# Kernel optimization log

Measured on AMD Instinct MI355X. Metric: run time of the kernel, lower is better.

## Reference

```python
import jax, jax.numpy as jnp
import numpy as np

N_NODES = 50000
N_EDGES = 800000
IN_DIM = 5
HID = (32, 64, 128, 64, 32)
OUT_DIM = 2
EPS = 1e-5  # nn.BatchNorm1d default eps


def _bn(x, g, b):
    # BatchNorm1d in training mode: batch (biased) statistics over nodes
    m = jnp.mean(x, axis=0)
    v = jnp.var(x, axis=0)
    return (x - m) * jax.lax.rsqrt(v + EPS) * g + b


def setup_inputs() -> dict:
    key = jax.random.key(0)
    ks = jax.random.split(key, 40)
    it = iter(range(40))
    def nrm(shape, s=0.1):
        return jax.random.normal(ks[next(it)], shape, jnp.float32) * s
    inp = {}
    inp["x"] = jax.random.normal(ks[next(it)], (N_NODES, IN_DIM), jnp.float32)
    inp["edge_index"] = jax.random.randint(ks[next(it)], (2, N_EDGES), 0, N_NODES, jnp.int32)
    # input embedding: Linear(5,32) -> ReLU -> BatchNorm1d(32)
    inp["emb_W"] = nrm((IN_DIM, HID[0]))
    inp["emb_b"] = jnp.zeros((HID[0],), jnp.float32)
    inp["emb_g"] = jnp.ones((HID[0],), jnp.float32)
    inp["emb_beta"] = jnp.zeros((HID[0],), jnp.float32)
    # 4 GraphConv blocks
    for i in range(len(HID) - 1):
        din, dout = HID[i], HID[i + 1]
        inp[f"b{i}_Wrel"] = nrm((din, dout))   # lin_rel weight (has bias)
        inp[f"b{i}_brel"] = jnp.zeros((dout,), jnp.float32)
        inp[f"b{i}_Wroot"] = nrm((din, dout))  # lin_root weight (no bias)
        inp[f"b{i}_g"] = jnp.ones((dout,), jnp.float32)
        inp[f"b{i}_beta"] = jnp.zeros((dout,), jnp.float32)
    # output MLP: Linear(32,16) -> ReLU -> Linear(16,2)
    inp["out_W1"] = nrm((HID[-1], HID[-1] // 2))
    inp["out_b1"] = jnp.zeros((HID[-1] // 2,), jnp.float32)
    inp["out_W2"] = nrm((HID[-1] // 2, OUT_DIM))
    inp["out_b2"] = jnp.zeros((OUT_DIM,), jnp.float32)
    return inp


def reference(x, edge_index,
              emb_W, emb_b, emb_g, emb_beta,
              b0_Wrel, b0_brel, b0_Wroot, b0_g, b0_beta,
              b1_Wrel, b1_brel, b1_Wroot, b1_g, b1_beta,
              b2_Wrel, b2_brel, b2_Wroot, b2_g, b2_beta,
              b3_Wrel, b3_brel, b3_Wroot, b3_g, b3_beta,
              out_W1, out_b1, out_W2, out_b2):
    src, dst = edge_index[0], edge_index[1]
    # input embedding: Linear -> ReLU -> BN
    h = jnp.maximum(x @ emb_W + emb_b, 0.0)
    h = _bn(h, emb_g, emb_beta)
    blocks = [
        (b0_Wrel, b0_brel, b0_Wroot, b0_g, b0_beta),
        (b1_Wrel, b1_brel, b1_Wroot, b1_g, b1_beta),
        (b2_Wrel, b2_brel, b2_Wroot, b2_g, b2_beta),
        (b3_Wrel, b3_brel, b3_Wroot, b3_g, b3_beta),
    ]
    for Wrel, brel, Wroot, g, beta in blocks:
        # GraphConv (aggr='add'): lin_rel(sum_{j in N(i)} x_j) + lin_root(x_i)
        agg = jax.ops.segment_sum(h[src], dst, num_segments=N_NODES)
        h = agg @ Wrel + brel + h @ Wroot
        # BN then ReLU (GNNBlock order)
        h = jnp.maximum(_bn(h, g, beta), 0.0)
    # output MLP
    h = jnp.maximum(h @ out_W1 + out_b1, 0.0)
    return h @ out_W2 + out_b2
```

## Files before the change

kernel.cpp:

```cpp
#include <hip/hip_runtime.h>

#define N_NODES 50000
#define N_EDGES 800000
#define BN_EPS 1e-5f

typedef unsigned int   u32;
typedef unsigned short u16;

__device__ __forceinline__ void fma4(float4& a, float s, const float4& w) {
    a.x += s * w.x; a.y += s * w.y; a.z += s * w.z; a.w += s * w.w;
}
__device__ __forceinline__ void add4(float4& a, const float4& b) {
    a.x += b.x; a.y += b.y; a.z += b.z; a.w += b.w;
}
__device__ __forceinline__ u16 f2bf(float f) {
    union { u32 i; float f; } c; c.f = f;
    return (u16)((c.i + 0x7FFFu + ((c.i >> 16) & 1u)) >> 16);
}
__device__ __forceinline__ float4 bf4(uint2 w) {
    union { u32 i; float f; } a, b, c, d;
    a.i = w.x << 16; b.i = w.x & 0xFFFF0000u;
    c.i = w.y << 16; d.i = w.y & 0xFFFF0000u;
    return make_float4(a.f, b.f, c.f, d.f);
}
__device__ __forceinline__ uint2 pack4(const float4& v) {
    uint2 w;
    w.x = (u32)f2bf(v.x) | ((u32)f2bf(v.y) << 16);
    w.y = (u32)f2bf(v.z) | ((u32)f2bf(v.w) << 16);
    return w;
}
__device__ __forceinline__ float bfx(const uint4& v, int kk) {
    u32 w = ((const u32*)&v)[kk >> 1];
    union { u32 i; float f; } c;
    c.i = (kk & 1) ? (w & 0xFFFF0000u) : (w << 16);
    return c.f;
}

template <int NY>
__device__ __forceinline__ bool xcd_decode(int nx, int& x, int& y) {
    const int s = blockIdx.x & (8 * NY - 1);
    const int g = blockIdx.x / (8 * NY);
    x = g * 8 + (s & 7);
    y = s >> 3;
    return x < nx;
}
static inline int xcd_grid(int nx, int ny) { return ((nx + 7) / 8 * 8) * ny; }

__global__ void zero_i(int* __restrict__ p, int n) {
    int i = blockIdx.x * blockDim.x + threadIdx.x;
    int stride = gridDim.x * blockDim.x;
    for (; i < n; i += stride) p[i] = 0;
}

__global__ void hist_kernel(const int* __restrict__ dst, int* __restrict__ cnt) {
    int i = blockIdx.x * blockDim.x + threadIdx.x;
    int stride = gridDim.x * blockDim.x;
    for (; i < N_EDGES; i += stride) atomicAdd(&cnt[dst[i]], 1);
}
__global__ void scan1_kernel(const int* __restrict__ cnt, int* __restrict__ rp,
                             int* __restrict__ bsum) {
    __shared__ int s[256];
    int t = threadIdx.x;
    int idx = blockIdx.x * 256 + t;
    int v = (idx < N_NODES) ? cnt[idx] : 0;
    s[t] = v;
    __syncthreads();
    for (int off = 1; off < 256; off <<= 1) {
        int x = 0;
        if (t >= off) x = s[t - off];
        __syncthreads();
        s[t] += x;
        __syncthreads();
    }
    if (idx < N_NODES) rp[idx] = s[t] - v;
    if (t == 255) bsum[blockIdx.x] = s[255];
}
__global__ void scan2_kernel(int* __restrict__ bsum, int nb, float* __restrict__ stats) {
    __shared__ int s[256];
    int t = threadIdx.x;
    for (int i = t; i < 5 * 256; i += 256) stats[i] = 0.f;
    int v = (t < nb) ? bsum[t] : 0;
    s[t] = v;
    __syncthreads();
    for (int off = 1; off < 256; off <<= 1) {
        int x = 0;
        if (t >= off) x = s[t - off];
        __syncthreads();
        s[t] += x;
        __syncthreads();
    }
    if (t < nb) bsum[t] = s[t] - v;
}
__global__ void scan3_kernel(int* __restrict__ rp, const int* __restrict__ bsum,
                             int* __restrict__ cnt) {
    int idx = blockIdx.x * 256 + threadIdx.x;
    if (idx < N_NODES) {
        rp[idx] += bsum[blockIdx.x];
        cnt[idx] = 0;
    }
    if (idx == 0) rp[N_NODES] = N_EDGES;
}
__global__ void fill_kernel(const int* __restrict__ src, const int* __restrict__ dst,
                            const int* __restrict__ rp, int* __restrict__ cur,
                            u16* __restrict__ ssrc) {
    int i = blockIdx.x * blockDim.x + threadIdx.x;
    int stride = gridDim.x * blockDim.x;
    for (; i < N_EDGES; i += stride) {
        int d = dst[i];
        int p = rp[d] + atomicAdd(&cur[d], 1);
        ssrc[p] = (u16)src[i];
    }
}

__global__ __launch_bounds__(256) void emb_fused(
    const float* __restrict__ x, const float* __restrict__ W,
    const float* __restrict__ b, u16* __restrict__ out16,
    float* __restrict__ stats) {
    __shared__ float lsum[32], lssq[32];
    if (threadIdx.x < 32) { lsum[threadIdx.x] = 0.f; lssq[threadIdx.x] = 0.f; }
    __syncthreads();
    const int o = threadIdx.x & 31;
    const int total = N_NODES * 32;
    float mys = 0.f, myq = 0.f;
    for (int base = blockIdx.x * 256; base < total; base += gridDim.x * 256) {
        int idx = base + threadIdx.x;
        float acc = 0.f;
        if (idx < total) {
            int n = idx >> 5;
            const float* xr = x + n * 5;
            acc = b[o];
#pragma unroll
            for (int k = 0; k < 5; ++k) acc += xr[k] * W[k * 32 + o];
            acc = fmaxf(acc, 0.f);
            out16[idx] = f2bf(acc);
        }
        mys += acc;
        myq += acc * acc;
    }
    mys += __shfl_xor(mys, 32);
    myq += __shfl_xor(myq, 32);
    if ((threadIdx.x & 63) < 32) { atomicAdd(&lsum[o], mys); atomicAdd(&lssq[o], myq); }
    __syncthreads();
    if (threadIdx.x < 32) {
        atomicAdd(&stats[threadIdx.x], lsum[threadIdx.x]);
        atomicAdd(&stats[32 + threadIdx.x], lssq[threadIdx.x]);
    }
}

template <int D>
__device__ __forceinline__ void bn_finalize_lds(
    const float* __restrict__ stats, const float* __restrict__ g,
    const float* __restrict__ beta, float* sc, float* sh) {
    const float invN = 1.f / (float)N_NODES;
    for (int f = threadIdx.x; f < D; f += 256) {
        float m = stats[f] * invN;
        float var = stats[D + f] * invN - m * m;
        float a = g[f] * rsqrtf(var + BN_EPS);
        sc[f] = a;
        sh[f] = beta[f] - m * a;
    }
    __syncthreads();
}

__global__ __launch_bounds__(256) void bn_apply16(
    const uint2* __restrict__ in16, u16* __restrict__ out16,
    const float* __restrict__ g, const float* __restrict__ beta,
    const float* __restrict__ stats, int logD) {
    const int D = 1 << logD;
    const int total4 = N_NODES << (logD - 2);
    const float invN = 1.f / (float)N_NODES;
    int idx = blockIdx.x * blockDim.x + threadIdx.x;
    int stride = gridDim.x * blockDim.x;
    for (; idx < total4; idx += stride) {
        int f = (idx & ((D >> 2) - 1)) << 2;
        float4 v = bf4(in16[idx]);
        float* vp = (float*)&v;
#pragma unroll
        for (int c = 0; c < 4; ++c) {
            float m = stats[f + c] * invN;
            float var = stats[D + f + c] * invN - m * m;
            vp[c] = fmaxf((vp[c] - m) * rsqrtf(var + BN_EPS) * g[f + c] + beta[f + c], 0.f);
        }
        ((uint2*)out16)[idx] = pack4(v);
    }
}

template <int LOGD>
__global__ __launch_bounds__(256) void gather_agg_bf16(
    const u16* __restrict__ h16, const int* __restrict__ rp,
    const u16* __restrict__ ssrc, uint2* __restrict__ agg16) {
    constexpr int QSH = LOGD - 2;
    int tid = blockIdx.x * 256 + threadIdx.x;
    int node = tid >> QSH;
    if (node >= N_NODES) return;
    int q = tid & ((1 << QSH) - 1);
    int e0 = rp[node], e1 = rp[node + 1];
    float4 acc = make_float4(0.f, 0.f, 0.f, 0.f);
    int e = e0;
    for (; e + 4 <= e1; e += 4) {
        int s0 = ssrc[e], s1 = ssrc[e + 1], s2 = ssrc[e + 2], s3 = ssrc[e + 3];
        uint2 w0 = ((const uint2*)(h16 + ((size_t)s0 << LOGD)))[q];
        uint2 w1 = ((const uint2*)(h16 + ((size_t)s1 << LOGD)))[q];
        uint2 w2 = ((const uint2*)(h16 + ((size_t)s2 << LOGD)))[q];
        uint2 w3 = ((const uint2*)(h16 + ((size_t)s3 << LOGD)))[q];
        float4 v0 = bf4(w0), v1 = bf4(w1), v2 = bf4(w2), v3 = bf4(w3);
        add4(v0, v1); add4(v2, v3); add4(acc, v0); add4(acc, v2);
    }
    for (; e < e1; ++e) {
        float4 v = bf4(((const uint2*)(h16 + ((size_t)ssrc[e] << LOGD)))[q]);
        add4(acc, v);
    }
    agg16[tid] = pack4(acc);
}

template <int DIN, int DOUT, int OBL, int NPT>
__global__ __launch_bounds__(256) void gconv_bn0(
    const u16* __restrict__ h16, const u16* __restrict__ agg16,
    const float* __restrict__ Wrel, const float* __restrict__ brel,
    const float* __restrict__ Wroot, u16* __restrict__ out16,
    const float* __restrict__ stats_in, const float* __restrict__ g_in,
    const float* __restrict__ beta_in, const int* __restrict__ deg,
    float* __restrict__ stats_out, int nx) {
    constexpr int NY = 2;
    constexpr int LPN = OBL / 4;
    constexpr int SLOTS = 256 / LPN;
    constexpr int KS = 8;
    constexpr int TOT4 = DIN * OBL / 4;
    int bx, by;
    if (!xcd_decode<NY>(nx, bx, by)) return;
    __shared__ __align__(16) float wl[2 * DIN * OBL];
    __shared__ __align__(16) float sc[DIN];
    __shared__ __align__(16) float sh[DIN];
    __shared__ float lsum[OBL], lssq[OBL];
    const int ob0 = by * OBL;
    for (int e4 = threadIdx.x; e4 < TOT4; e4 += 256) {
        int k = e4 / (OBL / 4);
        int j = (e4 % (OBL / 4)) * 4;
        ((float4*)wl)[e4] = *(const float4*)(Wrel + (size_t)k * DOUT + ob0 + j);
        ((float4*)wl)[TOT4 + e4] = *(const float4*)(Wroot + (size_t)k * DOUT + ob0 + j);
    }
    if (threadIdx.x < OBL) { lsum[threadIdx.x] = 0.f; lssq[threadIdx.x] = 0.f; }
    bn_finalize_lds<DIN>(stats_in, g_in, beta_in, sc, sh);

    const int q = threadIdx.x & (LPN - 1);
    const int slot = threadIdx.x / LPN;
    const int o0 = ob0 + q * 4;
    const int nbase = bx * (SLOTS * NPT) + slot;

    float degf[NPT];
#pragma unroll
    for (int i = 0; i < NPT; ++i) {
        int n = nbase + i * SLOTS;
        degf[i] = (n < N_NODES) ? (float)deg[n] : 0.f;
    }

    float4 bias = *(const float4*)(brel + o0);
    float4 acc[NPT];
#pragma unroll
    for (int i = 0; i < NPT; ++i) acc[i] = bias;

#pragma unroll 1
    for (int s = 0; s < DIN / KS; ++s) {
        const int k0 = s * KS;
        float4 s2[2] = {((const float4*)sc)[k0 / 4], ((const float4*)sc)[k0 / 4 + 1]};
        float4 t2[2] = {((const float4*)sh)[k0 / 4], ((const float4*)sh)[k0 / 4 + 1]};
        const float* scp = (const float*)s2;
        const float* shp = (const float*)t2;
        uint4 hv16[NPT], av16[NPT];
#pragma unroll
        for (int i = 0; i < NPT; ++i) {
            int n = nbase + i * SLOTS;
            int nn = (n < N_NODES) ? n : 0;
            hv16[i] = *(const uint4*)(h16 + (size_t)nn * DIN + k0);
            av16[i] = *(const uint4*)(agg16 + (size_t)nn * DIN + k0);
        }
#pragma unroll
        for (int kk = 0; kk < KS; ++kk) {
            float4 wr = *(const float4*)&wl[(k0 + kk) * OBL + q * 4];
            float4 wo = *(const float4*)&wl[DIN * OBL + (k0 + kk) * OBL + q * 4];
#pragma unroll
            for (int i = 0; i < NPT; ++i) {
                float a  = fmaf(bfx(av16[i], kk), scp[kk], degf[i] * shp[kk]);
                float hh = fmaf(bfx(hv16[i], kk), scp[kk], shp[kk]);
                fma4(acc[i], a, wr);
                fma4(acc[i], hh, wo);
            }
        }
    }
#pragma unroll
    for (int i = 0; i < NPT; ++i) {
        int n = nbase + i * SLOTS;
        if (n < N_NODES)
            *(uint2*)(out16 + (size_t)n * DOUT + o0) = pack4(acc[i]);
        else
            acc[i] = make_float4(0.f, 0.f, 0.f, 0.f);
    }
    float4 s4 = make_float4(0.f, 0.f, 0.f, 0.f);
    float4 q4 = make_float4(0.f, 0.f, 0.f, 0.f);
#pragma unroll
    for (int i = 0; i < NPT; ++i) {
        s4.x += acc[i].x; s4.y += acc[i].y; s4.z += acc[i].z; s4.w += acc[i].w;
        q4.x += acc[i].x * acc[i].x; q4.y += acc[i].y * acc[i].y;
        q4.z += acc[i].z * acc[i].z; q4.w += acc[i].w * acc[i].w;
    }
#pragma unroll
    for (int d = LPN; d < 64; d <<= 1) {
        s4.x += __shfl_xor(s4.x, d); s4.y += __shfl_xor(s4.y, d);
        s4.z += __shfl_xor(s4.z, d); s4.w += __shfl_xor(s4.w, d);
        q4.x += __shfl_xor(q4.x, d); q4.y += __shfl_xor(q4.y, d);
        q4.z += __shfl_xor(q4.z, d); q4.w += __shfl_xor(q4.w, d);
    }
    if ((threadIdx.x & 63) < LPN) {
        int c = q * 4;
        atomicAdd(&lsum[c + 0], s4.x); atomicAdd(&lsum[c + 1], s4.y);
        atomicAdd(&lsum[c + 2], s4.z); atomicAdd(&lsum[c + 3], s4.w);
        atomicAdd(&lssq[c + 0], q4.x); atomicAdd(&lssq[c + 1], q4.y);
        atomicAdd(&lssq[c + 2], q4.z); atomicAdd(&lssq[c + 3], q4.w);
    }
    __syncthreads();
    if (threadIdx.x < OBL) {
        atomicAdd(&stats_out[ob0 + threadIdx.x], lsum[threadIdx.x]);
        atomicAdd(&stats_out[DOUT + ob0 + threadIdx.x], lssq[threadIdx.x]);
    }
}

template <int DIN, int DOUT, int OBL, int NPT>
__global__ __launch_bounds__(256) void gconv_lds(
    const u16* __restrict__ h16, const u16* __restrict__ agg16,
    const float* __restrict__ Wrel, const float* __restrict__ brel,
    const float* __restrict__ Wroot, u16* __restrict__ out16,
    float* __restrict__ stats_out, int nx) {
    constexpr int NY = DOUT / OBL;
    constexpr int LPN = OBL / 4;
    constexpr int SLOTS = 256 / LPN;
    constexpr int KS = 8;
    constexpr int TOT4 = DIN * OBL / 4;
    int bx, by;
    if (!xcd_decode<NY>(nx, bx, by)) return;
    __shared__ __align__(16) float wl[2 * DIN * OBL];
    __shared__ float lsum[OBL], lssq[OBL];
    const int ob0 = by * OBL;
    for (int e4 = threadIdx.x; e4 < TOT4; e4 += 256) {
        int k = e4 / (OBL / 4);
        int j = (e4 % (OBL / 4)) * 4;
        ((float4*)wl)[e4] = *(const float4*)(Wrel + (size_t)k * DOUT + ob0 + j);
        ((float4*)wl)[TOT4 + e4] = *(const float4*)(Wroot + (size_t)k * DOUT + ob0 + j);
    }
    if (threadIdx.x < OBL) { lsum[threadIdx.x] = 0.f; lssq[threadIdx.x] = 0.f; }
    __syncthreads();

    const int q = threadIdx.x & (LPN - 1);
    const int slot = threadIdx.x / LPN;
    const int o0 = ob0 + q * 4;
    const int nbase = bx * (SLOTS * NPT) + slot;

    float4 bias = *(const float4*)(brel + o0);
    float4 acc[NPT];
#pragma unroll
    for (int i = 0; i < NPT; ++i) acc[i] = bias;

#pragma unroll 1
    for (int s = 0; s < DIN / KS; ++s) {
        const int k0 = s * KS;
        uint4 hv16[NPT], av16[NPT];
#pragma unroll
        for (int i = 0; i < NPT; ++i) {
            int n = nbase + i * SLOTS;
            int nn = (n < N_NODES) ? n : 0;
            hv16[i] = *(const uint4*)(h16 + (size_t)nn * DIN + k0);
            av16[i] = *(const uint4*)(agg16 + (size_t)nn * DIN + k0);
        }
#pragma unroll
        for (int kk = 0; kk < KS; ++kk) {
            float4 wr = *(const float4*)&wl[(k0 + kk) * OBL + q * 4];
            float4 wo = *(const float4*)&wl[DIN * OBL + (k0 + kk) * OBL + q * 4];
#pragma unroll
            for (int i = 0; i < NPT; ++i) {
                fma4(acc[i], bfx(av16[i], kk), wr);
                fma4(acc[i], bfx(hv16[i], kk), wo);
            }
        }
    }
#pragma unroll
    for (int i = 0; i < NPT; ++i) {
        int n = nbase + i * SLOTS;
        if (n < N_NODES)
            *(uint2*)(out16 + (size_t)n * DOUT + o0) = pack4(acc[i]);
        else
            acc[i] = make_float4(0.f, 0.f, 0.f, 0.f);
    }
    float4 s4 = make_float4(0.f, 0.f, 0.f, 0.f);
    float4 q4 = make_float4(0.f, 0.f, 0.f, 0.f);
#pragma unroll
    for (int i = 0; i < NPT; ++i) {
        s4.x += acc[i].x; s4.y += acc[i].y; s4.z += acc[i].z; s4.w += acc[i].w;
        q4.x += acc[i].x * acc[i].x; q4.y += acc[i].y * acc[i].y;
        q4.z += acc[i].z * acc[i].z; q4.w += acc[i].w * acc[i].w;
    }
#pragma unroll
    for (int d = LPN; d < 64; d <<= 1) {
        s4.x += __shfl_xor(s4.x, d); s4.y += __shfl_xor(s4.y, d);
        s4.z += __shfl_xor(s4.z, d); s4.w += __shfl_xor(s4.w, d);
        q4.x += __shfl_xor(q4.x, d); q4.y += __shfl_xor(q4.y, d);
        q4.z += __shfl_xor(q4.z, d); q4.w += __shfl_xor(q4.w, d);
    }
    if ((threadIdx.x & 63) < LPN) {
        int c = q * 4;
        atomicAdd(&lsum[c + 0], s4.x); atomicAdd(&lsum[c + 1], s4.y);
        atomicAdd(&lsum[c + 2], s4.z); atomicAdd(&lsum[c + 3], s4.w);
        atomicAdd(&lssq[c + 0], q4.x); atomicAdd(&lssq[c + 1], q4.y);
        atomicAdd(&lssq[c + 2], q4.z); atomicAdd(&lssq[c + 3], q4.w);
    }
    __syncthreads();
    if (threadIdx.x < OBL) {
        atomicAdd(&stats_out[ob0 + threadIdx.x], lsum[threadIdx.x]);
        atomicAdd(&stats_out[DOUT + ob0 + threadIdx.x], lssq[threadIdx.x]);
    }
}

template <int DIN, int DOUT, int OBL, int NPT>
__global__ __launch_bounds__(256) void prem_bn16(
    const u16* __restrict__ h16, const float* __restrict__ Wrel,
    const float* __restrict__ brel, const float* __restrict__ Wroot,
    u16* __restrict__ P16, float* __restrict__ Q,
    const float* __restrict__ stats_in, const float* __restrict__ g_in,
    const float* __restrict__ beta_in, int nx) {
    constexpr int NY = DOUT / OBL;
    constexpr int LPN = OBL / 4;
    constexpr int SLOTS = 256 / LPN;
    constexpr int KS = 8;
    constexpr int TOT4 = DIN * OBL / 4;
    int bx, by;
    if (!xcd_decode<NY>(nx, bx, by)) return;
    __shared__ __align__(16) float wl[2 * DIN * OBL];
    __shared__ __align__(16) float sc[DIN];
    __shared__ __align__(16) float sh[DIN];
    const int ob0 = by * OBL;
    for (int e4 = threadIdx.x; e4 < TOT4; e4 += 256) {
        int k = e4 / (OBL / 4);
        int j = (e4 % (OBL / 4)) * 4;
        ((float4*)wl)[e4] = *(const float4*)(Wrel + (size_t)k * DOUT + ob0 + j);
        ((float4*)wl)[TOT4 + e4] = *(const float4*)(Wroot + (size_t)k * DOUT + ob0 + j);
    }
    bn_finalize_lds<DIN>(stats_in, g_in, beta_in, sc, sh);

    const int q = threadIdx.x & (LPN - 1);
    const int slot = threadIdx.x / LPN;
    const int o0 = ob0 + q * 4;
    const int nbase = bx * (SLOTS * NPT) + slot;

    float4 bias = *(const float4*)(brel + o0);
    float4 accp[NPT], accq[NPT];
#pragma unroll
    for (int i = 0; i < NPT; ++i) {
        accp[i] = make_float4(0.f, 0.f, 0.f, 0.f);
        accq[i] = bias;
    }

#pragma unroll 1
    for (int s = 0; s < DIN / KS; ++s) {
        const int k0 = s * KS;
        float4 s2[2] = {((const float4*)sc)[k0 / 4], ((const float4*)sc)[k0 / 4 + 1]};
        float4 t2[2] = {((const float4*)sh)[k0 / 4], ((const float4*)sh)[k0 / 4 + 1]};
        const float* scp = (const float*)s2;
        const float* shp = (const float*)t2;
        uint4 hv16[NPT];
#pragma unroll
        for (int i = 0; i < NPT; ++i) {
            int n = nbase + i * SLOTS;
            int nn = (n < N_NODES) ? n : 0;
            hv16[i] = *(const uint4*)(h16 + (size_t)nn * DIN + k0);
        }
#pragma unroll
        for (int kk = 0; kk < KS; ++kk) {
            float4 wr = *(const float4*)&wl[(k0 + kk) * OBL + q * 4];
            float4 wo = *(const float4*)&wl[DIN * OBL + (k0 + kk) * OBL + q * 4];
#pragma unroll
            for (int i = 0; i < NPT; ++i) {
                float hh = fmaxf(fmaf(bfx(hv16[i], kk), scp[kk], shp[kk]), 0.f);
                fma4(accp[i], hh, wr);
                fma4(accq[i], hh, wo);
            }
        }
    }
#pragma unroll
    for (int i = 0; i < NPT; ++i) {
        int n = nbase + i * SLOTS;
        if (n < N_NODES) {
            *(uint2*)(P16 + (size_t)n * DOUT + o0) = pack4(accp[i]);
            *(float4*)(Q + (size_t)n * DOUT + o0) = accq[i];
        }
    }
}

template <int LOGD, int W16>
__global__ __launch_bounds__(256) void gather_add_bf16(
    const u16* __restrict__ P16, const int* __restrict__ rp,
    const u16* __restrict__ ssrc, float4* __restrict__ qio,
    u16* __restrict__ out16, float* __restrict__ stats) {
    constexpr int D = 1 << LOGD;
    constexpr int Q4 = D / 4;
    __shared__ float lsum[D], lssq[D];
    if (threadIdx.x < D) { lsum[threadIdx.x] = 0.f; lssq[threadIdx.x] = 0.f; }
    __syncthreads();

    const int total = N_NODES * Q4;
    const int q = threadIdx.x & (Q4 - 1);
    float4 mys = make_float4(0.f, 0.f, 0.f, 0.f);
    float4 myq = make_float4(0.f, 0.f, 0.f, 0.f);

    for (int base = blockIdx.x * 256; base < total; base += gridDim.x * 256) {
        int tid = base + threadIdx.x;
        float4 acc = make_float4(0.f, 0.f, 0.f, 0.f);
        if (tid < total) {
            int node = tid >> (LOGD - 2);
            int e0 = rp[node], e1 = rp[node + 1];
            acc = qio[tid];
            int e = e0;
            for (; e + 4 <= e1; e += 4) {
                int s0 = ssrc[e], s1 = ssrc[e + 1], s2 = ssrc[e + 2], s3 = ssrc[e + 3];
                uint2 w0 = ((const uint2*)(P16 + ((size_t)s0 << LOGD)))[q];
                uint2 w1 = ((const uint2*)(P16 + ((size_t)s1 << LOGD)))[q];
                uint2 w2 = ((const uint2*)(P16 + ((size_t)s2 << LOGD)))[q];
                uint2 w3 = ((const uint2*)(P16 + ((size_t)s3 << LOGD)))[q];
                float4 v0 = bf4(w0), v1 = bf4(w1), v2 = bf4(w2), v3 = bf4(w3);
                add4(v0, v1); add4(v2, v3); add4(acc, v0); add4(acc, v2);
            }
            for (; e < e1; ++e) {
                float4 v = bf4(((const uint2*)(P16 + ((size_t)ssrc[e] << LOGD)))[q]);
                add4(acc, v);
            }
            if (W16)
                ((uint2*)out16)[tid] = pack4(acc);
            else
                qio[tid] = acc;
        }
        mys.x += acc.x; mys.y += acc.y; mys.z += acc.z; mys.w += acc.w;
        myq.x += acc.x * acc.x; myq.y += acc.y * acc.y;
        myq.z += acc.z * acc.z; myq.w += acc.w * acc.w;
    }
#pragma unroll
    for (int d = Q4; d < 64; d <<= 1) {
        mys.x += __shfl_xor(mys.x, d); mys.y += __shfl_xor(mys.y, d);
        mys.z += __shfl_xor(mys.z, d); mys.w += __shfl_xor(mys.w, d);
        myq.x += __shfl_xor(myq.x, d); myq.y += __shfl_xor(myq.y, d);
        myq.z += __shfl_xor(myq.z, d); myq.w += __shfl_xor(myq.w, d);
    }
    if ((threadIdx.x & 63) < Q4) {
        atomicAdd(&lsum[4 * q + 0], mys.x); atomicAdd(&lsum[4 * q + 1], mys.y);
        atomicAdd(&lsum[4 * q + 2], mys.z); atomicAdd(&lsum[4 * q + 3], mys.w);
        atomicAdd(&lssq[4 * q + 0], myq.x); atomicAdd(&lssq[4 * q + 1], myq.y);
        atomicAdd(&lssq[4 * q + 2], myq.z); atomicAdd(&lssq[4 * q + 3], myq.w);
    }
    __syncthreads();
    if (threadIdx.x < D) {
        atomicAdd(&stats[threadIdx.x], lsum[threadIdx.x]);
        atomicAdd(&stats[D + threadIdx.x], lssq[threadIdx.x]);
    }
}

__global__ __launch_bounds__(256) void outmlp_kernel(
    const float* __restrict__ h, const float* __restrict__ stats,
    const float* __restrict__ g, const float* __restrict__ beta,
    const float* __restrict__ W1, const float* __restrict__ b1,
    const float* __restrict__ W2, const float* __restrict__ b2,
    float* __restrict__ out) {
    int n = blockIdx.x * 256 + threadIdx.x;
    if (n >= N_NODES) return;
    const float invN = 1.f / (float)N_NODES;
    const float4* hr4 = (const float4*)(h + (size_t)n * 32);
    float hv[32];
#pragma unroll
    for (int k4 = 0; k4 < 8; ++k4) {
        float4 v = hr4[k4];
        float* vp = (float*)&v;
#pragma unroll
        for (int c = 0; c < 4; ++c) {
            int f = 4 * k4 + c;
            float m = stats[f] * invN;
            float var = stats[32 + f] * invN - m * m;
            hv[f] = fmaxf((vp[c] - m) * rsqrtf(var + BN_EPS) * g[f] + beta[f], 0.f);
        }
    }
    float hid[16];
#pragma unroll
    for (int j = 0; j < 16; ++j) hid[j] = b1[j];
#pragma unroll
    for (int k = 0; k < 32; ++k) {
        float hk = hv[k];
#pragma unroll
        for (int j = 0; j < 16; ++j) hid[j] += hk * W1[k * 16 + j];
    }
    float o0 = b2[0], o1 = b2[1];
#pragma unroll
    for (int j = 0; j < 16; ++j) {
        float t = fmaxf(hid[j], 0.f);
        o0 += t * W2[j * 2 + 0];
        o1 += t * W2[j * 2 + 1];
    }
    out[n * 2 + 0] = o0;
    out[n * 2 + 1] = o1;
}

extern "C" void kernel_launch(void* const* d_in, const int* in_sizes, int n_in,
                              void* d_out, int out_size, void* d_ws, size_t ws_size,
                              hipStream_t stream) {
    const float* x        = (const float*)d_in[0];
    const int*   ei       = (const int*)d_in[1];
    const int*   src      = ei;
    const int*   dst      = ei + N_EDGES;
    const float* emb_W    = (const float*)d_in[2];
    const float* emb_b    = (const float*)d_in[3];
    const float* emb_g    = (const float*)d_in[4];
    const float* emb_beta = (const float*)d_in[5];
    const float* out_W1   = (const float*)d_in[26];
    const float* out_b1   = (const float*)d_in[27];
    const float* out_W2   = (const float*)d_in[28];
    const float* out_b2   = (const float*)d_in[29];

    float* ws = (float*)d_ws;
    float* q32   = ws;
    float* stats = ws + (size_t)N_NODES * 64;
    u16* h16emb = (u16*)(stats + 5 * 256);
    u16* AGG16  = h16emb + (size_t)N_NODES * 32;
    u16* r0_16  = AGG16 + (size_t)N_NODES * 64;
    u16* h16a   = r0_16 + (size_t)N_NODES * 64;
    u16* r1_16  = h16a + (size_t)N_NODES * 64;
    u16* h2_16  = r1_16 + (size_t)N_NODES * 128;
    int* rp     = (int*)(h2_16 + (size_t)N_NODES * 64);
    int* cnt    = rp + N_NODES + 1;
    int* bsum   = cnt + N_NODES;
    u16* ssrc   = (u16*)(bsum + 256);

    float* st0 = stats;
    float* st1 = stats + 256;
    float* st2 = stats + 512;
    float* st3 = stats + 768;
    float* st4 = stats + 1024;

    const int BS = 256;
    const int NB = (N_NODES + BS - 1) / BS;

    zero_i<<<64, BS, 0, stream>>>(cnt, N_NODES);
    hist_kernel<<<1024, BS, 0, stream>>>(dst, cnt);
    scan1_kernel<<<NB, 256, 0, stream>>>(cnt, rp, bsum);
    scan2_kernel<<<1, 256, 0, stream>>>(bsum, NB, stats);
    scan3_kernel<<<NB, 256, 0, stream>>>(rp, bsum, cnt);
    fill_kernel<<<1024, BS, 0, stream>>>(src, dst, rp, cnt, ssrc);

    emb_fused<<<512, BS, 0, stream>>>(x, emb_W, emb_b, h16emb, st0);

    gather_agg_bf16<5><<<(N_NODES * 8 + BS - 1) / BS, BS, 0, stream>>>(h16emb, rp, ssrc, (uint2*)AGG16);
    {
        const int nx = (N_NODES + 63) / 64;
        gconv_bn0<32, 64, 32, 2><<<xcd_grid(nx, 2), BS, 0, stream>>>(
            h16emb, AGG16, (const float*)d_in[6], (const float*)d_in[7], (const float*)d_in[8],
            r0_16, st0, emb_g, emb_beta, cnt, st1, nx);
    }
    bn_apply16<<<2048, BS, 0, stream>>>((const uint2*)r0_16, h16a,
                                        (const float*)d_in[9], (const float*)d_in[10], st1, 6);

    gather_agg_bf16<6><<<(N_NODES * 16 + BS - 1) / BS, BS, 0, stream>>>(h16a, rp, ssrc, (uint2*)AGG16);
    {
        const int nx = (N_NODES + 127) / 128;
        gconv_lds<64, 128, 32, 4><<<xcd_grid(nx, 4), BS, 0, stream>>>(
            h16a, AGG16, (const float*)d_in[11], (const float*)d_in[12], (const float*)d_in[13],
            r1_16, st2, nx);
    }

    {
        const int nx = (N_NODES + 127) / 128;
        prem_bn16<128, 64, 16, 2><<<xcd_grid(nx, 4), BS, 0, stream>>>(
            r1_16, (const float*)d_in[16], (const float*)d_in[17], (const float*)d_in[18],
            AGG16, q32, st2, (const float*)d_in[14], (const float*)d_in[15], nx);
    }
    gather_add_bf16<6, 1><<<512, BS, 0, stream>>>(AGG16, rp, ssrc, (float4*)q32, h2_16, st3);

    {
        const int nx = (N_NODES + 127) / 128;
        prem_bn16<64, 32, 16, 2><<<xcd_grid(nx, 2), BS, 0, stream>>>(
            h2_16, (const float*)d_in[21], (const float*)d_in[22], (const float*)d_in[23],
            AGG16, q32, st3, (const float*)d_in[19], (const float*)d_in[20], nx);
    }
    gather_add_bf16<5, 0><<<512, BS, 0, stream>>>(AGG16, rp, ssrc, (float4*)q32, (u16*)0, st4);

    outmlp_kernel<<<NB, BS, 0, stream>>>(
        q32, st4, (const float*)d_in[24], (const float*)d_in[25],
        out_W1, out_b1, out_W2, out_b2, (float*)d_out);
}
```

Baseline: 346.5 us.

## Fuse histogram with embedding kernel and enlarge gconv_bn0 row tile

Merges the edge-degree histogram and the input-embedding kernels into one launch, with disjoint block ranges doing each job, and moves the stats zeroing from scan2 into a combined zero kernel. The aim is to cut launch count and let the two independent jobs overlap on the GPU. It also changes gconv_bn0's template parameter from 2 to 4 and doubles the node tile from 64 to 128 rows, giving fewer, larger blocks. Risks: the gconv_bn0 tile change has to match the kernel's internal tiling assumptions, and the larger tile lowers the block count.

```diff
diff --git a/kernel.cpp b/kernel.cpp
--- a/kernel.cpp
+++ b/kernel.cpp
@@ -46,17 +46,59 @@
 }
 static inline int xcd_grid(int nx, int ny) { return ((nx + 7) / 8 * 8) * ny; }
 
-__global__ void zero_i(int* __restrict__ p, int n) {
-    int i = blockIdx.x * blockDim.x + threadIdx.x;
+__global__ void zero_all(int* __restrict__ cnt, float* __restrict__ stats) {
     int stride = gridDim.x * blockDim.x;
-    for (; i < n; i += stride) p[i] = 0;
-}
-
-__global__ void hist_kernel(const int* __restrict__ dst, int* __restrict__ cnt) {
-    int i = blockIdx.x * blockDim.x + threadIdx.x;
-    int stride = gridDim.x * blockDim.x;
-    for (; i < N_EDGES; i += stride) atomicAdd(&cnt[dst[i]], 1);
-}
+    for (int i = blockIdx.x * blockDim.x + threadIdx.x; i < N_NODES; i += stride)
+        cnt[i] = 0;
+    for (int i = blockIdx.x * blockDim.x + threadIdx.x; i < 5 * 256; i += stride)
+        stats[i] = 0.f;
+}
+
+#define HIST_BLOCKS 1024
+#define EMB_BLOCKS  512
+__global__ __launch_bounds__(256) void hist_emb_kernel(
+    const int* __restrict__ dst, int* __restrict__ cnt,
+    const float* __restrict__ x, const float* __restrict__ W,
+    const float* __restrict__ b, u16* __restrict__ out16,
+    float* __restrict__ stats) {
+    if (blockIdx.x < HIST_BLOCKS) {
+        int i = blockIdx.x * 256 + threadIdx.x;
+        int stride = HIST_BLOCKS * 256;
+        for (; i < N_EDGES; i += stride) atomicAdd(&cnt[dst[i]], 1);
+        return;
+    }
+    __shared__ float lsum[32], lssq[32];
+    if (threadIdx.x < 32) { lsum[threadIdx.x] = 0.f; lssq[threadIdx.x] = 0.f; }
+    __syncthreads();
+    const int o = threadIdx.x & 31;
+    const int total = N_NODES * 32;
+    const int ebid = blockIdx.x - HIST_BLOCKS;
+    float mys = 0.f, myq = 0.f;
+    for (int base = ebid * 256; base < total; base += EMB_BLOCKS * 256) {
+        int idx = base + threadIdx.x;
+        float acc = 0.f;
+        if (idx < total) {
+            int n = idx >> 5;
+            const float* xr = x + n * 5;
+            acc = b[o];
+#pragma unroll
+            for (int k = 0; k < 5; ++k) acc += xr[k] * W[k * 32 + o];
+            acc = fmaxf(acc, 0.f);
+            out16[idx] = f2bf(acc);
+        }
+        mys += acc;
+        myq += acc * acc;
+    }
+    mys += __shfl_xor(mys, 32);
+    myq += __shfl_xor(myq, 32);
+    if ((threadIdx.x & 63) < 32) { atomicAdd(&lsum[o], mys); atomicAdd(&lssq[o], myq); }
+    __syncthreads();
+    if (threadIdx.x < 32) {
+        atomicAdd(&stats[threadIdx.x], lsum[threadIdx.x]);
+        atomicAdd(&stats[32 + threadIdx.x], lssq[threadIdx.x]);
+    }
+}
+
 __global__ void scan1_kernel(const int* __restrict__ cnt, int* __restrict__ rp,
                              int* __restrict__ bsum) {
     __shared__ int s[256];
@@ -75,10 +117,9 @@
     if (idx < N_NODES) rp[idx] = s[t] - v;
     if (t == 255) bsum[blockIdx.x] = s[255];
 }
-__global__ void scan2_kernel(int* __restrict__ bsum, int nb, float* __restrict__ stats) {
+__global__ void scan2_kernel(int* __restrict__ bsum, int nb) {
     __shared__ int s[256];
     int t = threadIdx.x;
-    for (int i = t; i < 5 * 256; i += 256) stats[i] = 0.f;
     int v = (t < nb) ? bsum[t] : 0;
     s[t] = v;
     __syncthreads();
@@ -109,41 +150,6 @@
         int d = dst[i];
         int p = rp[d] + atomicAdd(&cur[d], 1);
         ssrc[p] = (u16)src[i];
-    }
-}
-
-__global__ __launch_bounds__(256) void emb_fused(
-    const float* __restrict__ x, const float* __restrict__ W,
-    const float* __restrict__ b, u16* __restrict__ out16,
-    float* __restrict__ stats) {
-    __shared__ float lsum[32], lssq[32];
-    if (threadIdx.x < 32) { lsum[threadIdx.x] = 0.f; lssq[threadIdx.x] = 0.f; }
-    __syncthreads();
-    const int o = threadIdx.x & 31;
-    const int total = N_NODES * 32;
-    float mys = 0.f, myq = 0.f;
-    for (int base = blockIdx.x * 256; base < total; base += gridDim.x * 256) {
-        int idx = base + threadIdx.x;
-        float acc = 0.f;
-        if (idx < total) {
-            int n = idx >> 5;
-            const float* xr = x + n * 5;
-            acc = b[o];
-#pragma unroll
-            for (int k = 0; k < 5; ++k) acc += xr[k] * W[k * 32 + o];
-            acc = fmaxf(acc, 0.f);
-            out16[idx] = f2bf(acc);
-        }
-        mys += acc;
-        myq += acc * acc;
-    }
-    mys += __shfl_xor(mys, 32);
-    myq += __shfl_xor(myq, 32);
-    if ((threadIdx.x & 63) < 32) { atomicAdd(&lsum[o], mys); atomicAdd(&lssq[o], myq); }
-    __syncthreads();
-    if (threadIdx.x < 32) {
-        atomicAdd(&stats[threadIdx.x], lsum[threadIdx.x]);
-        atomicAdd(&stats[32 + threadIdx.x], lssq[threadIdx.x]);
     }
 }
 
@@ -641,19 +647,19 @@
     const int BS = 256;
     const int NB = (N_NODES + BS - 1) / BS;
 
-    zero_i<<<64, BS, 0, stream>>>(cnt, N_NODES);
-    hist_kernel<<<1024, BS, 0, stream>>>(dst, cnt);
+    zero_all<<<64, BS, 0, stream>>>(cnt, stats);
+    hist_emb_kernel<<<HIST_BLOCKS + EMB_BLOCKS, BS, 0, stream>>>(
+        dst, cnt, x, emb_W, emb_b, h16emb, st0);
+
     scan1_kernel<<<NB, 256, 0, stream>>>(cnt, rp, bsum);
-    scan2_kernel<<<1, 256, 0, stream>>>(bsum, NB, stats);
+    scan2_kernel<<<1, 256, 0, stream>>>(bsum, NB);
     scan3_kernel<<<NB, 256, 0, stream>>>(rp, bsum, cnt);
     fill_kernel<<<1024, BS, 0, stream>>>(src, dst, rp, cnt, ssrc);
 
-    emb_fused<<<512, BS, 0, stream>>>(x, emb_W, emb_b, h16emb, st0);
-
     gather_agg_bf16<5><<<(N_NODES * 8 + BS - 1) / BS, BS, 0, stream>>>(h16emb, rp, ssrc, (uint2*)AGG16);
     {
-        const int nx = (N_NODES + 63) / 64;
-        gconv_bn0<32, 64, 32, 2><<<xcd_grid(nx, 2), BS, 0, stream>>>(
+        const int nx = (N_NODES + 127) / 128;
+        gconv_bn0<32, 64, 32, 4><<<xcd_grid(nx, 2), BS, 0, stream>>>(
             h16emb, AGG16, (const float*)d_in[6], (const float*)d_in[7], (const float*)d_in[8],
             r0_16, st0, emb_g, emb_beta, cnt, st1, nx);
     }
```

New measurement: 331.3 us. -4.4%, faster.
